# Optimization experiments

Hardware: AMD Instinct MI355X
Metric: run time of the kernel (lower is better)

The kernel has to match this reference:

```python
import jax, jax.numpy as jnp
import numpy as np

N_QUBITS = 4
N_SEL_LAYERS = 2  # StronglyEntanglingLayers depth; ranges default = (l % (n-1)) + 1


def _apply_1q_batched(state, gate, wire):
    # state: (B, 2,2,2,2) complex; gate: (B, 2, 2) complex, per-row gate
    s = jnp.moveaxis(state, wire + 1, -1)
    s = jnp.einsum('b...i,bji->b...j', s, gate)
    return jnp.moveaxis(s, -1, wire + 1)


def _apply_1q(state, gate, wire):
    # state: (B, 2,2,2,2); gate: (2, 2) shared across batch
    s = jnp.moveaxis(state, wire + 1, -1)
    s = s @ gate.T
    return jnp.moveaxis(s, -1, wire + 1)


def _cnot(state, c, t):
    # flip target axis where control bit == 1
    s = jnp.moveaxis(state, (c + 1, t + 1), (1, 2))
    s = jnp.concatenate([s[:, :1], jnp.flip(s[:, 1:], axis=2)], axis=1)
    return jnp.moveaxis(s, (1, 2), (c + 1, t + 1))


def _rot_gate(w):
    # PennyLane Rot(phi, theta, omega) = RZ(omega) RY(theta) RZ(phi)
    phi, theta, omega = w[0], w[1], w[2]
    c = jnp.cos(theta * 0.5)
    s = jnp.sin(theta * 0.5)
    g00 = jnp.exp(-0.5j * (phi + omega)) * c
    g01 = -jnp.exp(0.5j * (phi - omega)) * s
    g10 = jnp.exp(-0.5j * (phi - omega)) * s
    g11 = jnp.exp(0.5j * (phi + omega)) * c
    return jnp.stack([jnp.stack([g00, g01]), jnp.stack([g10, g11])])  # (2,2) complex64


def _qnode(inputs, weights):
    # inputs: (B, 4) angles; weights: (2, 4, 3). Returns <Z_0> per row, (B,)
    B = inputs.shape[0]
    state = jnp.zeros((B, 16), jnp.complex64).at[:, 0].set(1.0)
    state = state.reshape((B,) + (2,) * N_QUBITS)
    # AngleEmbedding: default rotation='X' -> RX(inputs[w]) on wire w
    half = 0.5 * inputs
    for w in range(N_QUBITS):
        c = jnp.cos(half[:, w]).astype(jnp.complex64)
        s = (-1j) * jnp.sin(half[:, w]).astype(jnp.complex64)
        gate = jnp.stack([jnp.stack([c, s], -1), jnp.stack([s, c], -1)], -2)  # (B,2,2)
        state = _apply_1q_batched(state, gate, w)
    # StronglyEntanglingLayers: Rot on each wire, then ring of CNOTs with range r
    for l in range(N_SEL_LAYERS):
        for w in range(N_QUBITS):
            state = _apply_1q(state, _rot_gate(weights[l, w]), w)
        r = (l % (N_QUBITS - 1)) + 1
        for w in range(N_QUBITS):
            state = _cnot(state, w, (w + r) % N_QUBITS)
    sr = state.reshape(B, 2, 8)
    p = jnp.sum(sr.real ** 2 + sr.imag ** 2, axis=-1)  # (B, 2) marginal of wire 0
    return p[:, 0] - p[:, 1]


def _quad(x, weights):
    # x: (B, N, F) with F % 4 == 0 -> flatten to 4-wide circuit rows (literal view(-1,4))
    B = x.shape[0]
    flat = x.reshape(-1, N_QUBITS)
    out = _qnode(flat, weights)
    return out.reshape(B, -1, 1)


def _regroup(x, h):
    # 'b (h w) c -> b c h w' then 'b c (h h2)(w w2) -> b (h w) (h2 w2 c)', h2=w2=2
    B, N, C = x.shape
    w = N // h
    x = x.reshape(B, h // 2, 2, w // 2, 2, C)
    x = x.transpose(0, 1, 3, 2, 4, 5)  # (B, h/2, w/2, h2, w2, C)
    return x.reshape(B, (h // 2) * (w // 2), 4 * C)


def setup_inputs() -> dict:
    key = jax.random.key(0)
    ks = jax.random.split(key, 8)
    B = 8192
    two_pi = float(2.0 * np.pi)
    x = jax.random.normal(ks[0], (B, 1, 32, 32), jnp.float32)
    We = jax.random.normal(ks[1], (16, 4), jnp.float32) * 0.25   # nn.Linear(16, 4)
    be = jnp.zeros((4,), jnp.float32)
    w1 = jax.random.uniform(ks[2], (2, 4, 3), jnp.float32, 0.0, two_pi)
    w2 = jax.random.uniform(ks[3], (2, 4, 3), jnp.float32, 0.0, two_pi)
    w3 = jax.random.uniform(ks[4], (2, 4, 3), jnp.float32, 0.0, two_pi)
    Wh = jax.random.normal(ks[5], (1, 10), jnp.float32)          # nn.Linear(1, 10)
    bh = jnp.zeros((10,), jnp.float32)
    return {"x": x, "We": We, "be": be, "w1": w1, "w2": w2, "w3": w3, "Wh": Wh, "bh": bh}


def reference(x, We, be, w1, w2, w3, Wh, bh):
    B = x.shape[0]
    # 'b c (h p1) (w p2) -> b (h w) (p1 p2 c)', p1=p2=4, c=1, img 32 -> 8x8 patches
    p = x.reshape(B, 1, 8, 4, 8, 4).transpose(0, 2, 4, 3, 5, 1).reshape(B, 64, 16)
    h = jnp.tanh(p @ We + be)  # (B, 64, 4)
    curr_h = 8
    for w in (w1, w2, w3):
        h = _regroup(h, curr_h)
        h = _quad(h, w)
        curr_h //= 2
    # head Linear(1, 10) applied on trailing singleton feature dim: (B, 4, 1) -> (B, 4, 10)
    return h @ Wh + bh
```

## Files before the change

kernel.cpp:

```cpp
#include <hip/hip_runtime.h>
#include <math.h>

#define NELEM 4

__device__ __forceinline__ void make_gate(float phi, float th, float om, float* g) {
  float ct, st, cp, sp, cm, sm;
  __sincosf(0.5f * th, &st, &ct);
  __sincosf(0.5f * (phi + om), &sp, &cp);
  __sincosf(0.5f * (phi - om), &sm, &cm);
  g[0] =  cp * ct; g[1] = -sp * ct;
  g[2] = -cm * st; g[3] = -sm * st;
  g[4] =  cm * st; g[5] = -sm * st;
  g[6] =  cp * ct; g[7] =  sp * ct;
}

__device__ __forceinline__ float fast_tanh(float x) {
  float e = __expf(2.0f * x);
  return __builtin_fmaf(-2.0f, __builtin_amdgcn_rcpf(e + 1.0f), 1.0f);
}

__device__ __forceinline__ float circuit18(float a0, float a1, float a2, float a3,
                                           const float* __restrict__ K) {
  float s0, c0, s1, c1, s2, c2, s3, c3;
  __sincosf(a0, &s0, &c0);
  __sincosf(a1, &s1, &c1);
  __sincosf(a2, &s2, &c2);
  __sincosf(a3, &s3, &c3);
  float t0  = K[0] * c0 + K[1] * s0;
  float t1  = K[2] * c1 + K[3] * s1;
  float t2  = K[4] * c2 + K[5] * s2;
  float k2r = K[6] + K[7] * c2 + K[8] * s2;
  float k2i = K[9] + K[10] * c2 + K[11] * s2;
  float k3r = K[12] + K[13] * c3 + K[14] * s3;
  float tt = t0 * t1;
  return K[15] * (tt * t2) + k3r * (K[16] * k2r + K[17] * (tt * k2i));
}

__global__ __launch_bounds__(256, 4) void fused_ttn(
    const float* __restrict__ x, const float* __restrict__ We,
    const float* __restrict__ be, const float* __restrict__ w1,
    const float* __restrict__ w2, const float* __restrict__ w3,
    const float* __restrict__ Wh, const float* __restrict__ bh,
    float* __restrict__ out, int B) {
  __shared__ __align__(16) float sC[3][20];
  __shared__ __align__(16) float sWe[64];
  __shared__ float sbe[4];
  __shared__ float sWh[10];
  __shared__ float sbh[10];
  __shared__ float qbuf[NELEM * 65];
  __shared__ float q2buf[NELEM * 17];
  __shared__ float e3buf[NELEM * 4];

  const int t = threadIdx.x;
  const int wv = t >> 6, lane = t & 63;
  const int ph = lane >> 3, pw = lane & 7;

  float4 xv[4];
  const float4* xb = (const float4*)x;
  size_t gb = (size_t)blockIdx.x * NELEM + wv;
  if (gb >= (size_t)B) gb = 0;
#pragma unroll
  for (int p1 = 0; p1 < 4; ++p1)
    xv[p1] = xb[gb * 256 + (ph * 4 + p1) * 8 + pw];

  if (t < 12) {
    int s = t >> 2, w = t & 3;
    const float* W = (s == 0) ? w1 : (s == 1) ? w2 : w3;
    float g[8];
    make_gate(W[w * 3], W[w * 3 + 1], W[w * 3 + 2], g);
    float* K = &sC[s][0];
    float Qt = g[0] * g[0] + g[1] * g[1] - g[4] * g[4] - g[5] * g[5];
    float Rt = (g[0] * g[3] - g[1] * g[2]) - (g[4] * g[7] - g[5] * g[6]);
    if (w < 2) {
      K[w * 2] = Qt; K[w * 2 + 1] = Rt;
    } else if (w == 2) {
      K[4] = Qt; K[5] = Rt;
      float u  = g[0] * g[4] + g[1] * g[5], v  = g[2] * g[6] + g[3] * g[7];
      float p  = g[0] * g[5] - g[1] * g[4], q  = g[2] * g[7] - g[3] * g[6];
      float r1 = g[2] * g[4] + g[3] * g[5], m1 = g[2] * g[5] - g[3] * g[4];
      float r2 = g[0] * g[6] + g[1] * g[7], m2 = g[0] * g[7] - g[1] * g[6];
      K[6] = 0.5f * (u + v);  K[7]  = 0.5f * (u - v);  K[8]  = 0.5f * (m2 - m1);
      K[9] = 0.5f * (p + q);  K[10] = 0.5f * (p - q);  K[11] = 0.5f * (r1 - r2);
    } else {
      float u  = g[0] * g[4] + g[1] * g[5], v  = g[2] * g[6] + g[3] * g[7];
      float m1 = g[2] * g[5] - g[3] * g[4], m2 = g[0] * g[7] - g[1] * g[6];
      K[12] = 0.5f * (u + v); K[13] = 0.5f * (u - v); K[14] = 0.5f * (m2 - m1);
    }
  } else if (t < 15) {
    int s = t - 12;
    const float* W = (s == 0) ? w1 : (s == 1) ? w2 : w3;
    float g[8];
    make_gate(W[18], W[19], W[20], g);
    float A    = g[0] * g[0] + g[1] * g[1] - g[4] * g[4] - g[5] * g[5];
    float M01r = g[0] * g[2] + g[1] * g[3] - (g[4] * g[6] + g[5] * g[7]);
    float M01i = (g[0] * g[3] - g[1] * g[2]) - (g[4] * g[7] - g[5] * g[6]);
    sC[s][15] = A; sC[s][16] = 4.0f * M01r; sC[s][17] = -4.0f * M01i;
  }
  if (t < 64) sWe[t] = We[t];
  if (t < 4)  sbe[t] = be[t];
  if (t < 10) { sWh[t] = Wh[t]; sbh[t] = bh[t]; }
  __syncthreads();

  const int grp = (ph >> 1) * 4 + (pw >> 1);
  const int sub = (ph & 1) * 2 + (pw & 1);
  float a0 = sbe[0], a1 = sbe[1], a2 = sbe[2], a3 = sbe[3];
#pragma unroll
  for (int p1 = 0; p1 < 4; ++p1) {
    float4 v = xv[p1];
    float vv[4] = {v.x, v.y, v.z, v.w};
#pragma unroll
    for (int p2 = 0; p2 < 4; ++p2) {
      int f = p1 * 4 + p2;
      a0 = __builtin_fmaf(vv[p2], sWe[f * 4 + 0], a0);
      a1 = __builtin_fmaf(vv[p2], sWe[f * 4 + 1], a1);
      a2 = __builtin_fmaf(vv[p2], sWe[f * 4 + 2], a2);
      a3 = __builtin_fmaf(vv[p2], sWe[f * 4 + 3], a3);
    }
  }
  float e1 = circuit18(fast_tanh(a0), fast_tanh(a1), fast_tanh(a2),
                       fast_tanh(a3), &sC[0][0]);
  qbuf[wv * 65 + grp * 4 + sub] = e1;
  __syncthreads();

  if (t < NELEM * 16) {
    int e2 = t >> 4, c = t & 15;
    int base = e2 * 65 + (c >> 3) * 32 + (c & 7) * 2;
    float r = circuit18(qbuf[base], qbuf[base + 1], qbuf[base + 16],
                        qbuf[base + 17], &sC[1][0]);
    q2buf[e2 * 17 + c] = r;
  }
  __syncthreads();

  if (t < NELEM * 4) {
    int e3 = t >> 2, c = t & 3;
    int base = e3 * 17 + c * 2;
    float r = circuit18(q2buf[base], q2buf[base + 1], q2buf[base + 8],
                        q2buf[base + 9], &sC[2][0]);
    e3buf[e3 * 4 + c] = r;
  }
  __syncthreads();

  if (t < NELEM * 40) {
    int eo = t / 40;
    int j  = t - eo * 40;
    int g3 = j / 10;
    int k  = j - g3 * 10;
    int b  = blockIdx.x * NELEM + eo;
    if (b < B) out[(size_t)blockIdx.x * (NELEM * 40) + t] =
        e3buf[eo * 4 + g3] * sWh[k] + sbh[k];
  }
}

extern "C" void kernel_launch(void* const* d_in, const int* in_sizes, int n_in,
                              void* d_out, int out_size, void* d_ws, size_t ws_size,
                              hipStream_t stream) {
  (void)n_in; (void)out_size; (void)d_ws; (void)ws_size;
  const float* x  = (const float*)d_in[0];
  const float* We = (const float*)d_in[1];
  const float* be = (const float*)d_in[2];
  const float* w1 = (const float*)d_in[3];
  const float* w2 = (const float*)d_in[4];
  const float* w3 = (const float*)d_in[5];
  const float* Wh = (const float*)d_in[6];
  const float* bh = (const float*)d_in[7];
  float* out = (float*)d_out;

  int B = in_sizes[0] / 1024;
  int blocks = (B + NELEM - 1) / NELEM;
  hipLaunchKernelGGL(fused_ttn, dim3(blocks), dim3(256), 0, stream,
                     x, We, be, w1, w2, w3, Wh, bh, out, B);
}
```

Baseline: 11.66 us.

## Replace shared-memory tree reduction stages with intra-wavefront shuffles

Each batch element's three circuit stages already live in one 64-lane wavefront, so the intermediate results are now exchanged with cross-lane shuffles instead of shared-memory buffers. This removes three block-wide barriers and the shared-memory round trips. Every wavefront writes its own 40 outputs. The launch-bounds occupancy hint is also raised from 4 to 8 blocks. In exchange, all lanes compute the redundant later stages, and the lane-index mapping has to match the earlier qbuf layout exactly.

```diff
diff --git a/kernel.cpp b/kernel.cpp
--- a/kernel.cpp
+++ b/kernel.cpp
@@ -36,7 +36,11 @@
   return K[15] * (tt * t2) + k3r * (K[16] * k2r + K[17] * (tt * k2i));
 }
 
-__global__ __launch_bounds__(256, 4) void fused_ttn(
+__device__ __forceinline__ int q1lane(int q) {
+  return ((q >> 4) << 4) | (((q >> 1) & 1) << 3) | (((q >> 2) & 3) << 1) | (q & 1);
+}
+
+__global__ __launch_bounds__(256, 8) void fused_ttn(
     const float* __restrict__ x, const float* __restrict__ We,
     const float* __restrict__ be, const float* __restrict__ w1,
     const float* __restrict__ w2, const float* __restrict__ w3,
@@ -47,9 +51,6 @@
   __shared__ float sbe[4];
   __shared__ float sWh[10];
   __shared__ float sbh[10];
-  __shared__ float qbuf[NELEM * 65];
-  __shared__ float q2buf[NELEM * 17];
-  __shared__ float e3buf[NELEM * 4];
 
   const int t = threadIdx.x;
   const int wv = t >> 6, lane = t & 63;
@@ -101,8 +102,6 @@
   if (t < 10) { sWh[t] = Wh[t]; sbh[t] = bh[t]; }
   __syncthreads();
 
-  const int grp = (ph >> 1) * 4 + (pw >> 1);
-  const int sub = (ph & 1) * 2 + (pw & 1);
   float a0 = sbe[0], a1 = sbe[1], a2 = sbe[2], a3 = sbe[3];
 #pragma unroll
   for (int p1 = 0; p1 < 4; ++p1) {
@@ -119,35 +118,32 @@
   }
   float e1 = circuit18(fast_tanh(a0), fast_tanh(a1), fast_tanh(a2),
                        fast_tanh(a3), &sC[0][0]);
-  qbuf[wv * 65 + grp * 4 + sub] = e1;
-  __syncthreads();
 
-  if (t < NELEM * 16) {
-    int e2 = t >> 4, c = t & 15;
-    int base = e2 * 65 + (c >> 3) * 32 + (c & 7) * 2;
-    float r = circuit18(qbuf[base], qbuf[base + 1], qbuf[base + 16],
-                        qbuf[base + 17], &sC[1][0]);
-    q2buf[e2 * 17 + c] = r;
+  {
+    int c = lane & 15;
+    int base = ((c >> 3) << 5) | ((c & 7) << 1);
+    float b0 = __shfl(e1, q1lane(base), 64);
+    float b1 = __shfl(e1, q1lane(base + 1), 64);
+    float b2 = __shfl(e1, q1lane(base + 16), 64);
+    float b3 = __shfl(e1, q1lane(base + 17), 64);
+    e1 = circuit18(b0, b1, b2, b3, &sC[1][0]);
   }
-  __syncthreads();
 
-  if (t < NELEM * 4) {
-    int e3 = t >> 2, c = t & 3;
-    int base = e3 * 17 + c * 2;
-    float r = circuit18(q2buf[base], q2buf[base + 1], q2buf[base + 8],
-                        q2buf[base + 9], &sC[2][0]);
-    e3buf[e3 * 4 + c] = r;
+  {
+    int d = lane & 3;
+    float b0 = __shfl(e1, d * 2, 64);
+    float b1 = __shfl(e1, d * 2 + 1, 64);
+    float b2 = __shfl(e1, d * 2 + 8, 64);
+    float b3 = __shfl(e1, d * 2 + 9, 64);
+    e1 = circuit18(b0, b1, b2, b3, &sC[2][0]);
   }
-  __syncthreads();
 
-  if (t < NELEM * 40) {
-    int eo = t / 40;
-    int j  = t - eo * 40;
-    int g3 = j / 10;
-    int k  = j - g3 * 10;
-    int b  = blockIdx.x * NELEM + eo;
-    if (b < B) out[(size_t)blockIdx.x * (NELEM * 40) + t] =
-        e3buf[eo * 4 + g3] * sWh[k] + sbh[k];
+  if (lane < 40) {
+    int g3 = lane / 10;
+    int k  = lane - g3 * 10;
+    float ev = __shfl(e1, g3, 64);
+    size_t b = (size_t)blockIdx.x * NELEM + wv;
+    if (b < (size_t)B) out[b * 40 + lane] = ev * sWh[k] + sbh[k];
   }
 }
 
```

New measurement: 11.72 us (median of 2 runs). Within noise of the previous version (+0.5%).
